# Kernel tuning notes

Hardware: AMD Instinct MI355X
Metric: run time of the kernel (lower is better)

Reference implementation:

```python
import jax, jax.numpy as jnp
import numpy as np
from jax import lax


def _conv2d(x, w, b):
    # x: [B,C,H,W], w: [O,I,3,3], 'SAME' padding, stride 1
    y = lax.conv_general_dilated(x, w, (1, 1), 'SAME',
                                 dimension_numbers=('NCHW', 'OIHW', 'NCHW'))
    return y + b[None, :, None, None]


def _grid_sample_border(img, grid):
    # img: [B,C,H,W]; grid: [B,H,W,2] with (x,y) in [-1,1]; align_corners=True,
    # bilinear, padding_mode='border' (coords clamped before interpolation).
    B, C, H, W = img.shape
    ix = jnp.clip((grid[..., 0] + 1.0) * (W - 1) / 2.0, 0.0, W - 1.0)
    iy = jnp.clip((grid[..., 1] + 1.0) * (H - 1) / 2.0, 0.0, H - 1.0)
    x0f = jnp.floor(ix)
    y0f = jnp.floor(iy)
    wx = (ix - x0f)[:, None]  # [B,1,H,W]
    wy = (iy - y0f)[:, None]
    x0 = jnp.clip(x0f.astype(jnp.int32), 0, W - 1)
    x1 = jnp.clip(x0 + 1, 0, W - 1)
    y0 = jnp.clip(y0f.astype(jnp.int32), 0, H - 1)
    y1 = jnp.clip(y0 + 1, 0, H - 1)
    flat = img.reshape(B, C, H * W)

    def gather(yi, xi):
        idx = (yi * W + xi).reshape(B, 1, H * W)
        g = jnp.take_along_axis(flat, jnp.broadcast_to(idx, (B, C, H * W)), axis=2)
        return g.reshape(B, C, H, W)

    v00 = gather(y0, x0)
    v01 = gather(y0, x1)
    v10 = gather(y1, x0)
    v11 = gather(y1, x1)
    top = v00 * (1.0 - wx) + v01 * wx
    bot = v10 * (1.0 - wx) + v11 * wx
    return top * (1.0 - wy) + bot * wy


def setup_inputs() -> dict:
    key = jax.random.key(0)
    ks = jax.random.split(key, 4)
    B, C, H, W = 4, 64, 256, 256
    z_real = jax.random.normal(ks[0], (B, C, H, W), dtype=jnp.float32)
    z_imag = jax.random.normal(ks[1], (B, C, H, W), dtype=jnp.float32)
    fan1 = C * 9
    w1 = jax.random.normal(ks[2], (64, C, 3, 3), dtype=jnp.float32) / np.sqrt(fan1)
    b1 = jnp.zeros((64,), dtype=jnp.float32)
    w2 = jax.random.normal(ks[3], (1, 64, 3, 3), dtype=jnp.float32) / np.sqrt(64 * 9)
    b2 = jnp.zeros((1,), dtype=jnp.float32)
    dt = jnp.float32(0.1)
    return {"z_real": z_real, "z_imag": z_imag, "dt": dt,
            "w1": w1, "b1": b1, "w2": w2, "b2": b2}


def reference(z_real, z_imag, dt, w1, b1, w2, b2):
    B, C, H, W = z_real.shape
    # psi_net: conv -> SiLU -> conv, scaled by dt; psi: [B,1,H,W]
    psi = _conv2d(jax.nn.silu(_conv2d(z_real, w1, b1)), w2, b2) * dt
    # curl with replicate padding, central differences
    p = jnp.pad(psi, ((0, 0), (0, 0), (1, 1), (1, 1)), mode='edge')
    u = (p[:, :, 2:, 1:-1] - p[:, :, :-2, 1:-1]) / 2.0
    v = -(p[:, :, 1:-1, 2:] - p[:, :, 1:-1, :-2]) / 2.0
    # normalized flow: [B,H,W,2]
    flow = jnp.concatenate([u / (W / 2.0), v / (H / 2.0)], axis=1).transpose(0, 2, 3, 1)
    yy, xx = jnp.meshgrid(jnp.linspace(-1.0, 1.0, H), jnp.linspace(-1.0, 1.0, W), indexing='ij')
    base = jnp.stack((xx, yy), axis=-1).astype(z_real.dtype)  # [H,W,2]
    sampling_grid = base[None] - flow
    # sample real and imag in one fused gather over 2C channels
    zc = jnp.concatenate([z_real, z_imag], axis=1)  # [B,2C,H,W]
    out = _grid_sample_border(zc, sampling_grid)
    return out  # [B,2C,H,W]: first C channels = real part, last C = imag part
```

## Files before the change

### kernel.cpp

```cpp
#include <hip/hip_runtime.h>
#include <cmath>

namespace {
constexpr int H = 256, W = 256, HWp = H * W;
constexpr size_t PLANE = (size_t)4 * HWp * 64 * 2;
constexpr size_t NEED_FAST = 73728 + 2 * PLANE + (1u << 20);
}

typedef _Float16 f16;
typedef unsigned int u32;
typedef __attribute__((ext_vector_type(4))) _Float16 f16x4;
typedef __attribute__((ext_vector_type(8))) _Float16 f16x8;
typedef __attribute__((ext_vector_type(4))) float f32x4;
typedef __attribute__((ext_vector_type(4))) unsigned int u32x4;

__device__ __forceinline__ void dma16(const char* g, char* l) {
    __builtin_amdgcn_global_load_lds(
        (const __attribute__((address_space(1))) u32*)g,
        (__attribute__((address_space(3))) u32*)l, 16, 0, 0);
}

__global__ void k_wt(const float* __restrict__ w1, f16* __restrict__ w1tb) {
    int i = blockIdx.x * 256 + threadIdx.x;
    if (i >= 64 * 576) return;
    int co = i / 576, r = i - co * 576;
    int ci = r / 9, k9 = r - ci * 9;
    w1tb[(k9 * 64 + co) * 64 + ci] = (f16)w1[i];
}

__global__ __launch_bounds__(256) void k_xt2(const float* __restrict__ zr,
                                             const float* __restrict__ zi,
                                             f16* __restrict__ Xt_r,
                                             f16* __restrict__ Xt_i) {
    __shared__ f16 tile[64][80];
    const int t = threadIdx.x;
    const int p0 = blockIdx.x * 64;
    const int bb = blockIdx.y & 3;
    const bool im = blockIdx.y >= 4;
    const float* x = im ? zi : zr;
    f16* dst = im ? Xt_i : Xt_r;
    const size_t base = (size_t)bb * 64 * HWp;
#pragma unroll
    for (int r = 0; r < 4; ++r) {
        int q = r * 256 + t;
        int ci = q >> 4, px4 = (q & 15) * 4;
        f32x4 v = *reinterpret_cast<const f32x4*>(x + base + (size_t)ci * HWp + p0 + px4);
#pragma unroll
        for (int j = 0; j < 4; ++j) tile[px4 + j][ci] = (f16)v[j];
    }
    __syncthreads();
    const int px = t >> 2, q = t & 3;
    u32x4* d = reinterpret_cast<u32x4*>(dst + ((size_t)bb * HWp + p0 + px) * 64 + q * 16);
    const u32x4* s = reinterpret_cast<const u32x4*>(&tile[px][q * 16]);
    d[0] = s[0];
    d[1] = s[1];
}

__global__ __launch_bounds__(256, 3) void k_conv1(
        const f16* __restrict__ Xt,
        const f16* __restrict__ w1tb,
        const float* __restrict__ b1,
        f16* __restrict__ act) {
    __shared__ __align__(16) char lds[18432];

    const int tid = threadIdx.x;
    const int lane = tid & 63, wid = tid >> 6;
    const int lr = lane & 15, lg = lane >> 4;
    const int wpx = wid & 1, wco = wid >> 1;

    const int bid = blockIdx.x;
    const int swz = (bid & 7) * 256 + (bid >> 3);
    const int b = swz >> 9;
    const int y = (swz >> 1) & 255;
    const int x0 = (swz & 1) << 7;

    const int swzb = (lane ^ ((lane >> 3) & 7)) << 4;

    f32x4 acc[4][2];
#pragma unroll
    for (int m = 0; m < 4; ++m)
#pragma unroll
        for (int n = 0; n < 2; ++n) acc[m][n] = (f32x4)0.f;

    const f16x8 zf = (f16x8)(f16)0.f;
    const f16* Wbase = w1tb + (size_t)(wco * 32 + lr) * 64 + lg * 8;

    for (int dyi = 0; dyi < 3; ++dyi) {
        const int yy = y + dyi - 1;
        if ((unsigned)yy >= 256u) continue;

        __syncthreads();
        {
            const char* asrc = (const char*)Xt +
                ((((size_t)b * 256 + yy) * 256 + x0 - 8) * 128) + swzb;
            for (int j = wid; j < 18; j += 4)
                dma16(asrc + j * 1024, lds + j * 1024);
        }
        __syncthreads();

#pragma unroll
        for (int kx = 0; kx < 3; ++kx) {
            const int dx = kx - 1;
            const int gx0 = x0 + wpx * 64 + lr + dx;
            const bool ok0 = (unsigned)gx0 < 256u;
            const bool ok3 = (unsigned)(gx0 + 48) < 256u;
            const int arow = (8 + wpx * 64 + lr + dx) << 7;
            const int axor = (lr + dx) & 7;
            const f16* Wk = Wbase + (size_t)(dyi * 3 + kx) * 4096;
#pragma unroll
            for (int c = 0; c < 2; ++c) {
                const int abase = arow + (((c * 4 + lg) ^ axor) << 4);
                f16x8 A0 = *reinterpret_cast<const f16x8*>(lds + abase);
                f16x8 A1 = *reinterpret_cast<const f16x8*>(lds + abase + 2048);
                f16x8 A2 = *reinterpret_cast<const f16x8*>(lds + abase + 4096);
                f16x8 A3 = *reinterpret_cast<const f16x8*>(lds + abase + 6144);
                const f16* Wc = Wk + c * 32;
                f16x8 W0 = *reinterpret_cast<const f16x8*>(Wc);
                f16x8 W1 = *reinterpret_cast<const f16x8*>(Wc + 1024);
                A0 = ok0 ? A0 : zf;
                A3 = ok3 ? A3 : zf;
                acc[0][0] = __builtin_amdgcn_mfma_f32_16x16x32_f16(W0, A0, acc[0][0], 0, 0, 0);
                acc[0][1] = __builtin_amdgcn_mfma_f32_16x16x32_f16(W1, A0, acc[0][1], 0, 0, 0);
                acc[1][0] = __builtin_amdgcn_mfma_f32_16x16x32_f16(W0, A1, acc[1][0], 0, 0, 0);
                acc[1][1] = __builtin_amdgcn_mfma_f32_16x16x32_f16(W1, A1, acc[1][1], 0, 0, 0);
                acc[2][0] = __builtin_amdgcn_mfma_f32_16x16x32_f16(W0, A2, acc[2][0], 0, 0, 0);
                acc[2][1] = __builtin_amdgcn_mfma_f32_16x16x32_f16(W1, A2, acc[2][1], 0, 0, 0);
                acc[3][0] = __builtin_amdgcn_mfma_f32_16x16x32_f16(W0, A3, acc[3][0], 0, 0, 0);
                acc[3][1] = __builtin_amdgcn_mfma_f32_16x16x32_f16(W1, A3, acc[3][1], 0, 0, 0);
            }
        }
    }

    float bias[2][4];
#pragma unroll
    for (int n = 0; n < 2; ++n) {
        f32x4 bv = *reinterpret_cast<const f32x4*>(b1 + wco * 32 + n * 16 + lg * 4);
#pragma unroll
        for (int r = 0; r < 4; ++r) bias[n][r] = bv[r];
    }
    const size_t row_base = ((size_t)b * 256 + y) * 256;
#pragma unroll
    for (int m = 0; m < 4; ++m) {
        f16* ap = act + (row_base + x0 + wpx * 64 + m * 16 + lr) * 64 + wco * 32 + lg * 4;
#pragma unroll
        for (int n = 0; n < 2; ++n) {
            f16x4 o;
#pragma unroll
            for (int r = 0; r < 4; ++r) {
                float v = acc[m][n][r] + bias[n][r];
                v = v / (1.f + __expf(-v));
                o[r] = (f16)v;
            }
            *reinterpret_cast<f16x4*>(ap + n * 16) = o;
        }
    }
}

__global__ __launch_bounds__(256) void k_conv2(
        const f16* __restrict__ act, const float* __restrict__ w2,
        const float* __restrict__ b2, const float* __restrict__ dtp,
        float* __restrict__ psi) {
    const int tx = threadIdx.x & 31, ty = threadIdx.x >> 5;
    const int px = blockIdx.x * 32 + tx;
    const int py = blockIdx.y * 8 + ty;
    const int b = blockIdx.z;

    float a0 = 0.f, a1 = 0.f, a2 = 0.f, a3 = 0.f;
#pragma unroll
    for (int dy = -1; dy <= 1; ++dy) {
        const int yy = py + dy;
        if ((unsigned)yy >= (unsigned)H) continue;
#pragma unroll
        for (int dx = -1; dx <= 1; ++dx) {
            const int xx = px + dx;
            const int k9 = (dy + 1) * 3 + (dx + 1);
            if ((unsigned)xx < (unsigned)W) {
                const f16x8* ap = reinterpret_cast<const f16x8*>(
                    act + (((size_t)b * H + yy) * W + xx) * 64);
                const float* wp = w2 + k9;
#pragma unroll
                for (int g = 0; g < 8; ++g) {
                    const f16x8 v = ap[g];
                    const int cb = g * 8;
                    a0 = fmaf((float)v[0], wp[(cb + 0) * 9], a0);
                    a1 = fmaf((float)v[1], wp[(cb + 1) * 9], a1);
                    a2 = fmaf((float)v[2], wp[(cb + 2) * 9], a2);
                    a3 = fmaf((float)v[3], wp[(cb + 3) * 9], a3);
                    a0 = fmaf((float)v[4], wp[(cb + 4) * 9], a0);
                    a1 = fmaf((float)v[5], wp[(cb + 5) * 9], a1);
                    a2 = fmaf((float)v[6], wp[(cb + 6) * 9], a2);
                    a3 = fmaf((float)v[7], wp[(cb + 7) * 9], a3);
                }
            }
        }
    }
    psi[((size_t)b * H + py) * W + px] = ((a0 + a1) + (a2 + a3) + b2[0]) * dtp[0];
}

__global__ __launch_bounds__(256, 4) void k_sample3(
        const f16* __restrict__ Xt_r, const f16* __restrict__ Xt_i,
        const float* __restrict__ psi, float* __restrict__ out) {
    __shared__ int   s_off[4][128];
    __shared__ float s_w[4][128];
    __shared__ __align__(16) float s_stage[64][132];

    const int tid = threadIdx.x;
    const int bid = blockIdx.x;
    const int swz = (bid & 7) * 256 + (bid >> 3);
    const int seg = swz & 1, y = (swz >> 1) & 255, b = swz >> 9;
    const int x0 = seg * 128;

    if (tid < 128) {
        const int px = x0 + tid;
        const float* pb = psi + b * HWp;
        const int yp = min(y + 1, H - 1), ym = max(y - 1, 0);
        const int xp = min(px + 1, W - 1), xm = max(px - 1, 0);
        const float u = 0.5f * (pb[yp * W + px] - pb[ym * W + px]);
        const float v = -0.5f * (pb[y * W + xp] - pb[y * W + xm]);
        const float gx = (-1.f + 2.f * px / (float)(W - 1)) - u * (2.f / (float)W);
        const float gy = (-1.f + 2.f * y / (float)(H - 1)) - v * (2.f / (float)H);
        float ix = fminf(fmaxf((gx + 1.f) * 0.5f * (float)(W - 1), 0.f), (float)(W - 1));
        float iy = fminf(fmaxf((gy + 1.f) * 0.5f * (float)(H - 1), 0.f), (float)(H - 1));
        const float xf = floorf(ix), yf = floorf(iy);
        const float wx = ix - xf, wy = iy - yf;
        const int ix0 = (int)xf, iy0 = (int)yf;
        const int ix1 = min(ix0 + 1, W - 1), iy1 = min(iy0 + 1, H - 1);
        s_off[0][tid] = (iy0 * W + ix0) * 128;
        s_off[1][tid] = (iy0 * W + ix1) * 128;
        s_off[2][tid] = (iy1 * W + ix0) * 128;
        s_off[3][tid] = (iy1 * W + ix1) * 128;
        s_w[0][tid] = (1.f - wx) * (1.f - wy);
        s_w[1][tid] = wx * (1.f - wy);
        s_w[2][tid] = (1.f - wx) * wy;
        s_w[3][tid] = wx * wy;
    }
    __syncthreads();

    const int p = tid >> 1, s = tid & 1;
    const int o0 = s_off[0][p], o1 = s_off[1][p], o2 = s_off[2][p], o3 = s_off[3][p];
    const float w0 = s_w[0][p], w1 = s_w[1][p], w2 = s_w[2][p], w3 = s_w[3][p];
    const int cl = tid >> 5;
    const int pxq = (tid & 31) * 4;
    const size_t obase = (size_t)b * 128 * HWp + (size_t)y * W + x0 + pxq;

#pragma unroll
    for (int pl = 0; pl < 2; ++pl) {
        const char* base = (const char*)(pl ? Xt_i : Xt_r)
                         + (size_t)b * HWp * 128 + s * 64;
        const char* c0 = base + o0;
        const char* c1 = base + o1;
        const char* c2 = base + o2;
        const char* c3 = base + o3;
        f16x8 h00 = *(const f16x8*)(c0);      f16x8 h01 = *(const f16x8*)(c0 + 16);
        f16x8 h02 = *(const f16x8*)(c0 + 32); f16x8 h03 = *(const f16x8*)(c0 + 48);
        f16x8 h10 = *(const f16x8*)(c1);      f16x8 h11 = *(const f16x8*)(c1 + 16);
        f16x8 h12 = *(const f16x8*)(c1 + 32); f16x8 h13 = *(const f16x8*)(c1 + 48);
        f16x8 h20 = *(const f16x8*)(c2);      f16x8 h21 = *(const f16x8*)(c2 + 16);
        f16x8 h22 = *(const f16x8*)(c2 + 32); f16x8 h23 = *(const f16x8*)(c2 + 48);
        f16x8 h30 = *(const f16x8*)(c3);      f16x8 h31 = *(const f16x8*)(c3 + 16);
        f16x8 h32 = *(const f16x8*)(c3 + 32); f16x8 h33 = *(const f16x8*)(c3 + 48);

        const int rb = s << 5;
#pragma unroll
        for (int k = 0; k < 8; ++k) {
            s_stage[rb + k][p] = w0 * (float)h00[k] + w1 * (float)h10[k]
                               + w2 * (float)h20[k] + w3 * (float)h30[k];
            s_stage[rb + 8 + k][p] = w0 * (float)h01[k] + w1 * (float)h11[k]
                                   + w2 * (float)h21[k] + w3 * (float)h31[k];
            s_stage[rb + 16 + k][p] = w0 * (float)h02[k] + w1 * (float)h12[k]
                                    + w2 * (float)h22[k] + w3 * (float)h32[k];
            s_stage[rb + 24 + k][p] = w0 * (float)h03[k] + w1 * (float)h13[k]
                                    + w2 * (float)h23[k] + w3 * (float)h33[k];
        }
        __syncthreads();
#pragma unroll
        for (int k = 0; k < 8; ++k) {
            const int c = cl + (k << 3);
            f32x4 vv = *(const f32x4*)&s_stage[c][pxq];
            *(f32x4*)(out + obase + (size_t)(pl * 64 + c) * HWp) = vv;
        }
        __syncthreads();
    }
}

__global__ __launch_bounds__(256) void k_sample_fb(
        const float* __restrict__ zr, const float* __restrict__ zi,
        const float* __restrict__ psi, float* __restrict__ out) {
    const int tx = threadIdx.x & 31, ty = threadIdx.x >> 5;
    const int px = blockIdx.x * 32 + tx;
    const int py = blockIdx.y * 8 + ty;
    const int b  = blockIdx.z >> 3;
    const int c0 = (blockIdx.z & 7) * 16;

    const float* pb = psi + b * HWp;
    const int yp = min(py + 1, H - 1), ym = max(py - 1, 0);
    const int xp = min(px + 1, W - 1), xm = max(px - 1, 0);
    const float u = 0.5f * (pb[yp * W + px] - pb[ym * W + px]);
    const float v = -0.5f * (pb[py * W + xp] - pb[py * W + xm]);

    const float gx = (-1.f + 2.f * px / (float)(W - 1)) - u * (2.f / (float)W);
    const float gy = (-1.f + 2.f * py / (float)(H - 1)) - v * (2.f / (float)H);

    float ix = fminf(fmaxf((gx + 1.f) * 0.5f * (float)(W - 1), 0.f), (float)(W - 1));
    float iy = fminf(fmaxf((gy + 1.f) * 0.5f * (float)(H - 1), 0.f), (float)(H - 1));
    const float xf = floorf(ix), yf = floorf(iy);
    const float wx = ix - xf, wy = iy - yf;
    const int ix0 = (int)xf, iy0 = (int)yf;
    const int ix1 = min(ix0 + 1, W - 1), iy1 = min(iy0 + 1, H - 1);

    const int o00 = iy0 * W + ix0, o01 = iy0 * W + ix1;
    const int o10 = iy1 * W + ix0, o11 = iy1 * W + ix1;
    const float w00 = (1.f - wx) * (1.f - wy), w01 = wx * (1.f - wy);
    const float w10 = (1.f - wx) * wy, w11 = wx * wy;

    const float* src0 = (c0 < 64) ? (zr + (size_t)b * 64 * HWp + (size_t)c0 * HWp)
                                  : (zi + (size_t)b * 64 * HWp + (size_t)(c0 - 64) * HWp);
    float* ob = out + ((size_t)b * 128 + c0) * HWp + py * W + px;
#pragma unroll
    for (int c = 0; c < 16; ++c) {
        const float* p = src0 + (size_t)c * HWp;
        ob[(size_t)c * HWp] = p[o00] * w00 + p[o01] * w01 + p[o10] * w10 + p[o11] * w11;
    }
}

extern "C" void kernel_launch(void* const* d_in, const int* in_sizes, int n_in,
                              void* d_out, int out_size, void* d_ws, size_t ws_size,
                              hipStream_t stream) {
    const float* z_real = (const float*)d_in[0];
    const float* z_imag = (const float*)d_in[1];
    const float* dt     = (const float*)d_in[2];
    const float* w1     = (const float*)d_in[3];
    const float* b1     = (const float*)d_in[4];
    const float* w2     = (const float*)d_in[5];
    const float* b2     = (const float*)d_in[6];

    float* out = (float*)d_out;
    char* ws = (char*)d_ws;
    f16* w1tb = (f16*)ws;

    hipLaunchKernelGGL(k_wt, dim3(144), dim3(256), 0, stream, w1, w1tb);

    if (ws_size >= NEED_FAST) {
        f16* Xt_r  = (f16*)(ws + 73728);
        f16* Xt_i  = (f16*)(ws + 73728 + PLANE);
        float* psi = (float*)(ws + 73728 + 2 * PLANE);
        f16* act   = (f16*)d_out;

        hipLaunchKernelGGL(k_xt2, dim3(HWp / 64, 8), dim3(256), 0, stream,
                           z_real, z_imag, Xt_r, Xt_i);
        hipLaunchKernelGGL(k_conv1, dim3(2048), dim3(256), 0, stream, Xt_r, w1tb, b1, act);
        hipLaunchKernelGGL(k_conv2, dim3(8, 32, 4), dim3(256), 0, stream, act, w2, b2, dt, psi);
        hipLaunchKernelGGL(k_sample3, dim3(2048), dim3(256), 0, stream,
                           Xt_r, Xt_i, psi, out);
    } else {
        float* psi = (float*)(ws + 73728);
        f16* Xt  = (f16*)((char*)d_out + 4096);
        f16* act = (f16*)((char*)d_out + 4096 + PLANE);

        hipLaunchKernelGGL(k_xt2, dim3(HWp / 64, 4), dim3(256), 0, stream,
                           z_real, z_real, Xt, Xt);
        hipLaunchKernelGGL(k_conv1, dim3(2048), dim3(256), 0, stream, Xt, w1tb, b1, act);
        hipLaunchKernelGGL(k_conv2, dim3(8, 32, 4), dim3(256), 0, stream, act, w2, b2, dt, psi);
        hipLaunchKernelGGL(k_sample_fb, dim3(8, 32, 32), dim3(256), 0, stream,
                           z_real, z_imag, psi, out);
    }
}
```

Measured before the change: 171.8 us.

## Preload conv1 weights into registers and fold weight transpose into xt kernel

```diff
diff --git a/kernel.cpp b/kernel.cpp
--- a/kernel.cpp
+++ b/kernel.cpp
@@ -20,18 +20,22 @@
         (__attribute__((address_space(3))) u32*)l, 16, 0, 0);
 }
 
-__global__ void k_wt(const float* __restrict__ w1, f16* __restrict__ w1tb) {
-    int i = blockIdx.x * 256 + threadIdx.x;
-    if (i >= 64 * 576) return;
-    int co = i / 576, r = i - co * 576;
-    int ci = r / 9, k9 = r - ci * 9;
-    w1tb[(k9 * 64 + co) * 64 + ci] = (f16)w1[i];
-}
-
 __global__ __launch_bounds__(256) void k_xt2(const float* __restrict__ zr,
                                              const float* __restrict__ zi,
                                              f16* __restrict__ Xt_r,
-                                             f16* __restrict__ Xt_i) {
+                                             f16* __restrict__ Xt_i,
+                                             const float* __restrict__ w1,
+                                             f16* __restrict__ w1tb,
+                                             int ny_xt) {
+    if ((int)blockIdx.y == ny_xt) {
+        int i = blockIdx.x * 256 + threadIdx.x;
+        if (i < 64 * 576) {
+            int co = i / 576, r = i - co * 576;
+            int ci = r / 9, k9 = r - ci * 9;
+            w1tb[(k9 * 64 + co) * 64 + ci] = (f16)w1[i];
+        }
+        return;
+    }
     __shared__ f16 tile[64][80];
     const int t = threadIdx.x;
     const int p0 = blockIdx.x * 64;
@@ -56,7 +60,7 @@
     d[1] = s[1];
 }
 
-__global__ __launch_bounds__(256, 3) void k_conv1(
+__global__ __launch_bounds__(256, 2) void k_conv1(
         const f16* __restrict__ Xt,
         const f16* __restrict__ w1tb,
         const float* __restrict__ b1,
@@ -76,6 +80,17 @@
 
     const int swzb = (lane ^ ((lane >> 3) & 7)) << 4;
 
+    f16x8 Wreg[9][2][2];
+#pragma unroll
+    for (int k9 = 0; k9 < 9; ++k9)
+#pragma unroll
+        for (int n = 0; n < 2; ++n)
+#pragma unroll
+            for (int c = 0; c < 2; ++c)
+                Wreg[k9][n][c] = *reinterpret_cast<const f16x8*>(
+                    w1tb + (size_t)(k9 * 64 + wco * 32 + n * 16 + lr) * 64
+                         + c * 32 + lg * 8);
+
     f32x4 acc[4][2];
 #pragma unroll
     for (int m = 0; m < 4; ++m)
@@ -83,8 +98,8 @@
         for (int n = 0; n < 2; ++n) acc[m][n] = (f32x4)0.f;
 
     const f16x8 zf = (f16x8)(f16)0.f;
-    const f16* Wbase = w1tb + (size_t)(wco * 32 + lr) * 64 + lg * 8;
-
+
+#pragma unroll
     for (int dyi = 0; dyi < 3; ++dyi) {
         const int yy = y + dyi - 1;
         if ((unsigned)yy >= 256u) continue;
@@ -93,8 +108,11 @@
         {
             const char* asrc = (const char*)Xt +
                 ((((size_t)b * 256 + yy) * 256 + x0 - 8) * 128) + swzb;
-            for (int j = wid; j < 18; j += 4)
-                dma16(asrc + j * 1024, lds + j * 1024);
+#pragma unroll
+            for (int j = 0; j < 5; ++j) {
+                const int jj = wid + j * 4;
+                if (jj < 18) dma16(asrc + jj * 1024, lds + jj * 1024);
+            }
         }
         __syncthreads();
 
@@ -106,7 +124,6 @@
             const bool ok3 = (unsigned)(gx0 + 48) < 256u;
             const int arow = (8 + wpx * 64 + lr + dx) << 7;
             const int axor = (lr + dx) & 7;
-            const f16* Wk = Wbase + (size_t)(dyi * 3 + kx) * 4096;
 #pragma unroll
             for (int c = 0; c < 2; ++c) {
                 const int abase = arow + (((c * 4 + lg) ^ axor) << 4);
@@ -114,11 +131,10 @@
                 f16x8 A1 = *reinterpret_cast<const f16x8*>(lds + abase + 2048);
                 f16x8 A2 = *reinterpret_cast<const f16x8*>(lds + abase + 4096);
                 f16x8 A3 = *reinterpret_cast<const f16x8*>(lds + abase + 6144);
-                const f16* Wc = Wk + c * 32;
-                f16x8 W0 = *reinterpret_cast<const f16x8*>(Wc);
-                f16x8 W1 = *reinterpret_cast<const f16x8*>(Wc + 1024);
                 A0 = ok0 ? A0 : zf;
                 A3 = ok3 ? A3 : zf;
+                const f16x8 W0 = Wreg[dyi * 3 + kx][0][c];
+                const f16x8 W1 = Wreg[dyi * 3 + kx][1][c];
                 acc[0][0] = __builtin_amdgcn_mfma_f32_16x16x32_f16(W0, A0, acc[0][0], 0, 0, 0);
                 acc[0][1] = __builtin_amdgcn_mfma_f32_16x16x32_f16(W1, A0, acc[0][1], 0, 0, 0);
                 acc[1][0] = __builtin_amdgcn_mfma_f32_16x16x32_f16(W0, A1, acc[1][0], 0, 0, 0);
@@ -338,16 +354,14 @@
     char* ws = (char*)d_ws;
     f16* w1tb = (f16*)ws;
 
-    hipLaunchKernelGGL(k_wt, dim3(144), dim3(256), 0, stream, w1, w1tb);
-
     if (ws_size >= NEED_FAST) {
         f16* Xt_r  = (f16*)(ws + 73728);
         f16* Xt_i  = (f16*)(ws + 73728 + PLANE);
         float* psi = (float*)(ws + 73728 + 2 * PLANE);
         f16* act   = (f16*)d_out;
 
-        hipLaunchKernelGGL(k_xt2, dim3(HWp / 64, 8), dim3(256), 0, stream,
-                           z_real, z_imag, Xt_r, Xt_i);
+        hipLaunchKernelGGL(k_xt2, dim3(HWp / 64, 9), dim3(256), 0, stream,
+                           z_real, z_imag, Xt_r, Xt_i, w1, w1tb, 8);
         hipLaunchKernelGGL(k_conv1, dim3(2048), dim3(256), 0, stream, Xt_r, w1tb, b1, act);
         hipLaunchKernelGGL(k_conv2, dim3(8, 32, 4), dim3(256), 0, stream, act, w2, b2, dt, psi);
         hipLaunchKernelGGL(k_sample3, dim3(2048), dim3(256), 0, stream,
@@ -357,8 +371,8 @@
         f16* Xt  = (f16*)((char*)d_out + 4096);
         f16* act = (f16*)((char*)d_out + 4096 + PLANE);
 
-        hipLaunchKernelGGL(k_xt2, dim3(HWp / 64, 4), dim3(256), 0, stream,
-                           z_real, z_real, Xt, Xt);
+        hipLaunchKernelGGL(k_xt2, dim3(HWp / 64, 5), dim3(256), 0, stream,
+                           z_real, z_real, Xt, Xt, w1, w1tb, 4);
         hipLaunchKernelGGL(k_conv1, dim3(2048), dim3(256), 0, stream, Xt, w1tb, b1, act);
         hipLaunchKernelGGL(k_conv2, dim3(8, 32, 4), dim3(256), 0, stream, act, w2, b2, dt, psi);
         hipLaunchKernelGGL(k_sample_fb, dim3(8, 32, 32), dim3(256), 0, stream,
```

After: 169.6 us. No clear change (-1.3%).
